# Kernel optimization log

Measured on AMD Instinct MI355X. Metric: run time of the kernel, lower is better.

Reference implementation:

```python
import jax, jax.numpy as jnp
import numpy as np

B, TT, C, H, T = 4, 4096, 1024, 16, 128
K = C // H  # head size (rk and v head sizes equal here)
HEAD_DIV = 8.0  # head_size_divisor
EPS = 1e-5  # GroupNorm eps
LAYER_ID, N_LAYER = 12, 24


def setup_inputs() -> dict:
    key = jax.random.key(0)
    ks = jax.random.split(key, 8)
    r01 = LAYER_ID / (N_LAYER - 1)
    r1a0 = 1.0 - LAYER_ID / N_LAYER
    ddd = (jnp.arange(C, dtype=jnp.float32) / C).reshape(1, 1, C)
    h = jnp.arange(H, dtype=jnp.float32)
    scale = 0.02
    return {
        "xq": jax.random.normal(ks[0], (B, TT, C), jnp.float32),
        "time_mix_k": ddd ** r1a0,
        "time_mix_v": ddd ** r1a0 + 0.3 * r01,
        "time_mix_r": ddd ** (0.5 * r1a0),
        "time_mix_g": ddd ** (0.5 * r1a0),
        "time_decay": -8.0 + 7.0 * (h / (H - 1)) ** (0.7 + 1.3 * r01),
        "time_faaaa": r01 * (1.0 - h / (H - 1)),
        "W_r": jax.random.normal(ks[1], (C, C), jnp.float32) * scale,
        "W_k": jax.random.normal(ks[2], (C, C), jnp.float32) * scale,
        "W_v": jax.random.normal(ks[3], (C, C), jnp.float32) * scale,
        "W_g": jax.random.normal(ks[4], (C, C), jnp.float32) * scale,
        "W_o": jax.random.normal(ks[5], (C, C), jnp.float32) * scale,
        "ln_w": jnp.ones((C,), jnp.float32),
        "ln_b": jnp.zeros((C,), jnp.float32),
    }


def reference(xq, time_mix_k, time_mix_v, time_mix_r, time_mix_g,
              time_decay, time_faaaa, W_r, W_k, W_v, W_g, W_o, ln_w, ln_b):
    x = xq
    B_, TT_, C_ = x.shape
    N = TT_ // T  # number of chunks
    # time shift: xx[:, t] = x[:, t-1], xx[:, 0] = 0
    xx = jnp.pad(x, ((0, 0), (1, 0), (0, 0)))[:, :-1]
    xr = x * time_mix_r + xx * (1 - time_mix_r)
    xk = x * time_mix_k + xx * (1 - time_mix_k)
    xv = x * time_mix_v + xx * (1 - time_mix_v)
    xg = x * time_mix_g + xx * (1 - time_mix_g)
    r = (xr @ W_r.T).reshape(B_, TT_, H, K).transpose(0, 2, 1, 3)  # (B,H,TT,K)
    k = (xk @ W_k.T).reshape(B_, TT_, H, K).transpose(0, 2, 1, 3)
    v = (xv @ W_v.T).reshape(B_, TT_, H, K).transpose(0, 2, 1, 3)
    g = jax.nn.silu(xg @ W_g.T)  # (B,TT,C)

    decay = jnp.exp(-jnp.exp(time_decay))  # (H,)
    u = time_faaaa  # (H,)
    ws = decay ** T  # per-chunk state decay (H,)
    i_idx = jnp.arange(T)
    wb = decay[:, None] ** i_idx                # (H,T): decay^i
    wk = decay[:, None] ** (T - 1 - i_idx)      # (H,T): decay^(T-1-j)
    diff = i_idx[:, None] - i_idx[None, :]      # i - j
    pw = decay[:, None, None] ** jnp.maximum(diff - 1, 0)
    # lower-triangular intra-chunk decay: decay^(i-j-1) for i>j, u on diag
    w_mat = jnp.where(diff > 0, pw, 0.0) + jnp.eye(T, dtype=x.dtype) * u[:, None, None]  # (H,T,T)

    # chunked layout: (N, B, H, T, K)
    rc = r.reshape(B_, H, N, T, K).transpose(2, 0, 1, 3, 4)
    kc = k.reshape(B_, H, N, T, K).transpose(2, 0, 1, 3, 4)
    vc = v.reshape(B_, H, N, T, K).transpose(2, 0, 1, 3, 4)
    s0 = jnp.zeros((B_, H, K, K), x.dtype)

    def step(s, chunk):
        rr, kk, vv = chunk
        att = jnp.einsum('bhik,bhjk->bhij', rr, kk) * w_mat
        out = att @ vv + jnp.einsum('bhik,bhkv->bhiv', rr, s) * wb[None, :, :, None]
        s_new = ws[None, :, None, None] * s + jnp.einsum(
            'bhjk,bhjv->bhkv', kk * wk[None, :, :, None], vv)
        return s_new, out

    _, xo = jax.lax.scan(step, s0, (rc, kc, vc))  # xo: (N,B,H,T,K)
    xo = xo.transpose(1, 0, 3, 2, 4).reshape(B_, TT_, H, K)

    # GroupNorm(H groups) over channels, applied to x / head_size_divisor
    y = xo / HEAD_DIV
    mu = y.mean(-1, keepdims=True)
    var = y.var(-1, keepdims=True)
    y = (y - mu) / jnp.sqrt(var + EPS)
    y = y * ln_w.reshape(H, K) + ln_b.reshape(H, K)
    y = y.reshape(B_, TT_, C_)
    return (y * g) @ W_o.T
```

## Files before the change

kernel.cpp:

```cpp
#include <hip/hip_runtime.h>
#include <hip/hip_bf16.h>
#include <stdint.h>

#define C_DIM 1024
#define H_DIM 16
#define K_DIM 64
#define T_CH 128
#define TT_DIM 4096
#define B_DIM 4
#define N_CH 32
#define M_ROWS 16384

typedef __attribute__((ext_vector_type(8))) __bf16 bf16x8;
typedef __attribute__((ext_vector_type(4))) float floatx4;

__device__ __forceinline__ float bf2f(ushort u) {
  union { uint32_t i; float f; } v; v.i = ((uint32_t)u) << 16; return v.f;
}
__device__ __forceinline__ ushort f2bf(float f) {
  union { float f; uint32_t i; } v; v.f = f;
  return (ushort)((v.i + 0x7fffu + ((v.i >> 16) & 1u)) >> 16);
}

#define GLOAD_LDS16(g, l)                                                     \
  __builtin_amdgcn_global_load_lds(                                           \
      (const __attribute__((address_space(1))) void*)(g),                     \
      (__attribute__((address_space(3))) void*)(l), 16, 0, 0)

__global__ __launch_bounds__(256) void mix_kernel(
    const float* __restrict__ x,
    const float* __restrict__ mk, const float* __restrict__ mv,
    const float* __restrict__ mr, const float* __restrict__ mg,
    ushort* __restrict__ xr, ushort* __restrict__ xk,
    ushort* __restrict__ xv, ushort* __restrict__ xg) {
  long idx = (long)blockIdx.x * 256 + threadIdx.x;
  long e = idx * 4;
  int c = (int)(e & (C_DIM - 1));
  long row = e >> 10;
  int t = (int)(row & (TT_DIM - 1));
  floatx4 xc = *(const floatx4*)(x + e);
  floatx4 xp = {0.f, 0.f, 0.f, 0.f};
  if (t != 0) xp = *(const floatx4*)(x + e - C_DIM);
  floatx4 d = xc - xp;
  floatx4 vk = *(const floatx4*)(mk + c);
  floatx4 vv = *(const floatx4*)(mv + c);
  floatx4 vr = *(const floatx4*)(mr + c);
  floatx4 vg = *(const floatx4*)(mg + c);
  floatx4 ok = xp + d * vk;
  floatx4 ov = xp + d * vv;
  floatx4 orr = xp + d * vr;
  floatx4 og = xp + d * vg;
  union { ushort u[4]; uint2 q; } pk;
#define ST(dst, val)                                                          \
  pk.u[0] = f2bf(val.x); pk.u[1] = f2bf(val.y);                               \
  pk.u[2] = f2bf(val.z); pk.u[3] = f2bf(val.w);                               \
  *(uint2*)((dst) + e) = pk.q;
  ST(xk, ok) ST(xv, ov) ST(xr, orr) ST(xg, og)
#undef ST
}

__global__ __launch_bounds__(256) void wconv_kernel(
    const float* __restrict__ w0, const float* __restrict__ w1,
    const float* __restrict__ w2, const float* __restrict__ w3,
    const float* __restrict__ w4, ushort* __restrict__ o) {
  long idx = (long)blockIdx.x * 256 + threadIdx.x;
  long e = idx * 4;
  int wi = (int)(e >> 20);
  long off = e & ((1L << 20) - 1);
  const float* src = wi == 0 ? w0 : wi == 1 ? w1 : wi == 2 ? w2 : wi == 3 ? w3 : w4;
  floatx4 vv = *(const floatx4*)(src + off);
  union { ushort u[4]; uint2 q; } pk;
  pk.u[0] = f2bf(vv.x); pk.u[1] = f2bf(vv.y);
  pk.u[2] = f2bf(vv.z); pk.u[3] = f2bf(vv.w);
  *(uint2*)(o + e) = pk.q;
}

template <int EPI>
__global__ __launch_bounds__(256) void gemm_bt(
    const ushort* __restrict__ A, const ushort* __restrict__ Bt,
    void* __restrict__ Cout) {
  __shared__ __align__(16) ushort As[2][128 * 32];
  __shared__ __align__(16) ushort Bs[2][128 * 32];
  int tid = threadIdx.x;
  int lane = tid & 63, w = tid >> 6;
  int q = lane >> 4, l16 = lane & 15;
  int wm = w >> 1, wn = w & 1;
  int id = blockIdx.x;
  int bn = (id >> 3) & 7;
  int bm = (id & 7) | ((id >> 6) << 3);

  const ushort* gA0 = A + (long)(bm * 128 + w * 16 + (lane >> 2)) * C_DIM + (lane & 3) * 8;
  const ushort* gA1 = gA0 + 64 * C_DIM;
  const ushort* gB0 = Bt + (long)(bn * 128 + w * 16 + (lane >> 2)) * C_DIM + (lane & 3) * 8;
  const ushort* gB1 = gB0 + 64 * C_DIM;
  ushort* lA0 = As[0] + (w * 16) * 32;
  ushort* lA1 = As[0] + (64 + w * 16) * 32;
  ushort* lB0 = Bs[0] + (w * 16) * 32;
  ushort* lB1 = Bs[0] + (64 + w * 16) * 32;
  ushort* lA0p = As[1] + (w * 16) * 32;
  ushort* lA1p = As[1] + (64 + w * 16) * 32;
  ushort* lB0p = Bs[1] + (w * 16) * 32;
  ushort* lB1p = Bs[1] + (64 + w * 16) * 32;

  floatx4 acc[4][4] = {};

  for (int k0 = 0; k0 < C_DIM; k0 += 64) {
    __syncthreads();
    GLOAD_LDS16(gA0, lA0);
    GLOAD_LDS16(gA1, lA1);
    GLOAD_LDS16(gB0, lB0);
    GLOAD_LDS16(gB1, lB1);
    GLOAD_LDS16(gA0 + 32, lA0p);
    GLOAD_LDS16(gA1 + 32, lA1p);
    GLOAD_LDS16(gB0 + 32, lB0p);
    GLOAD_LDS16(gB1 + 32, lB1p);
    gA0 += 64; gA1 += 64; gB0 += 64; gB1 += 64;
    __syncthreads();
#pragma unroll
    for (int p = 0; p < 2; p++) {
      bf16x8 af[4], bfv[4];
#pragma unroll
      for (int i = 0; i < 4; i++)
        af[i] = *(const bf16x8*)&As[p][(wm * 64 + i * 16 + l16) * 32 + q * 8];
#pragma unroll
      for (int i = 0; i < 4; i++)
        bfv[i] = *(const bf16x8*)&Bs[p][(wn * 64 + i * 16 + l16) * 32 + q * 8];
#pragma unroll
      for (int mi = 0; mi < 4; mi++)
#pragma unroll
        for (int ni = 0; ni < 4; ni++)
          acc[mi][ni] = __builtin_amdgcn_mfma_f32_16x16x32_bf16(
              af[mi], bfv[ni], acc[mi][ni], 0, 0, 0);
    }
  }

  int row0 = bm * 128 + wm * 64 + q * 4;
  int col0 = bn * 128 + wn * 64 + l16;
#pragma unroll
  for (int mi = 0; mi < 4; mi++)
#pragma unroll
    for (int ni = 0; ni < 4; ni++)
#pragma unroll
      for (int rg = 0; rg < 4; rg++) {
        long off = (long)(row0 + mi * 16 + rg) * C_DIM + col0 + ni * 16;
        float val = acc[mi][ni][rg];
        if (EPI == 1) val = val / (1.f + expf(-val));
        if (EPI == 2)
          ((float*)Cout)[off] = val;
        else
          ((ushort*)Cout)[off] = f2bf(val);
      }
}

__global__ __launch_bounds__(256) void chunk_state(
    const ushort* __restrict__ kB, const ushort* __restrict__ vB,
    const float* __restrict__ td, ushort* __restrict__ Zc) {
  __shared__ __align__(16) ushort vt_s[64 * 136];
  __shared__ __align__(16) ushort kwt_s[64 * 136];
  int blk = blockIdx.x;
  int bh = blk >> 5, n = blk & 31;
  int b = bh >> 4, h = bh & 15;
  int tid = threadIdx.x;
  int lane = tid & 63, w = tid >> 6;
  int q = lane >> 4, l16 = lane & 15;
  float etd = expf(td[h]);
  long cbase = ((long)b * TT_DIM + n * T_CH) * C_DIM + h * K_DIM;

#pragma unroll
  for (int it = 0; it < 4; it++) {
    int chunk = it * 256 + tid;
    int row = chunk >> 3;
    int cc = (chunk & 7) * 8;
    long ga = cbase + (long)row * C_DIM + cc;
    uint4 kv4 = *(const uint4*)(kB + ga);
    uint4 vv4 = *(const uint4*)(vB + ga);
    float wkj = expf(-(float)(T_CH - 1 - row) * etd);
    const ushort* kp = (const ushort*)&kv4;
    const ushort* vp = (const ushort*)&vv4;
#pragma unroll
    for (int e2 = 0; e2 < 8; e2++) {
      kwt_s[(cc + e2) * 136 + row] = f2bf(bf2f(kp[e2]) * wkj);
      vt_s[(cc + e2) * 136 + row] = vp[e2];
    }
  }
  __syncthreads();

  floatx4 accZ[4] = {};
#pragma unroll
  for (int js = 0; js < 128; js += 32) {
    bf16x8 av = *(const bf16x8*)&vt_s[(w * 16 + l16) * 136 + q * 8 + js];
    bf16x8 bk3[4];
#pragma unroll
    for (int kt = 0; kt < 4; kt++)
      bk3[kt] = *(const bf16x8*)&kwt_s[(kt * 16 + l16) * 136 + q * 8 + js];
#pragma unroll
    for (int kt = 0; kt < 4; kt++)
      accZ[kt] = __builtin_amdgcn_mfma_f32_16x16x32_bf16(av, bk3[kt], accZ[kt], 0, 0, 0);
  }
  long zbase = (long)blk * 4096;
#pragma unroll
  for (int kt = 0; kt < 4; kt++)
#pragma unroll
    for (int rg = 0; rg < 4; rg++)
      Zc[zbase + (w * 16 + q * 4 + rg) * 64 + kt * 16 + l16] = f2bf(accZ[kt][rg]);
}

__global__ __launch_bounds__(256) void state_scan(
    const ushort* __restrict__ Zc, const float* __restrict__ td,
    ushort* __restrict__ Sb) {
  long tg = (long)blockIdx.x * 256 + threadIdx.x;
  int bh = (int)(tg >> 12);
  int e = (int)(tg & 4095);
  int h = bh & 15;
  float wsf = expf(-128.f * expf(td[h]));
  float s = 0.f;
  long base = (long)bh * N_CH * 4096 + e;
#pragma unroll
  for (int n = 0; n < N_CH; n++) {
    Sb[base + n * 4096] = f2bf(s);
    s = wsf * s + bf2f(Zc[base + n * 4096]);
  }
}

__global__ __launch_bounds__(256) void chunk_out(
    const ushort* __restrict__ rB, const ushort* __restrict__ kB,
    const ushort* __restrict__ vB, const ushort* __restrict__ gBuf,
    const ushort* __restrict__ Sb,
    const float* __restrict__ td, const float* __restrict__ tf,
    const float* __restrict__ lnw, const float* __restrict__ lnb,
    ushort* __restrict__ gy) {
  __shared__ __align__(16) ushort rr_s[128 * 72];
  __shared__ __align__(16) ushort un_s[128 * 136];
  __shared__ __align__(16) ushort vt_s[64 * 136];
  __shared__ __align__(16) ushort z_s[64 * 72];

  int blk = blockIdx.x;
  int bh = blk >> 5, n = blk & 31;
  int b = bh >> 4, h = bh & 15;
  int tid = threadIdx.x;
  int lane = tid & 63, w = tid >> 6;
  int q = lane >> 4, l16 = lane & 15;

  float etd = expf(td[h]);
  float u = tf[h];
  long cbase = ((long)b * TT_DIM + n * T_CH) * C_DIM + h * K_DIM;

#pragma unroll
  for (int it = 0; it < 4; it++) {
    int chunk = it * 256 + tid;
    int row = chunk >> 3;
    int cc = (chunk & 7) * 8;
    long ga = cbase + (long)row * C_DIM + cc;
    *(uint4*)&rr_s[row * 72 + cc] = *(const uint4*)(rB + ga);
    *(uint4*)&un_s[row * 136 + cc] = *(const uint4*)(kB + ga);
    uint4 vv4 = *(const uint4*)(vB + ga);
    const ushort* vp = (const ushort*)&vv4;
#pragma unroll
    for (int e2 = 0; e2 < 8; e2++) vt_s[(cc + e2) * 136 + row] = vp[e2];
  }
  {
    long sbase = (long)blk * 4096;
    int v = tid >> 2, c0 = (tid & 3) * 16;
    *(uint4*)&z_s[v * 72 + c0] = *(const uint4*)(Sb + sbase + v * 64 + c0);
    *(uint4*)&z_s[v * 72 + c0 + 8] = *(const uint4*)(Sb + sbase + v * 64 + c0 + 8);
  }
  __syncthreads();

  floatx4 accA[4][4] = {};
  int ai0 = (w >> 1) * 64, aj0 = (w & 1) * 64;
#pragma unroll
  for (int ks = 0; ks < 64; ks += 32) {
    bf16x8 af[4], bk2[4];
#pragma unroll
    for (int i = 0; i < 4; i++)
      af[i] = *(const bf16x8*)&rr_s[(ai0 + i * 16 + l16) * 72 + q * 8 + ks];
#pragma unroll
    for (int j = 0; j < 4; j++)
      bk2[j] = *(const bf16x8*)&un_s[(aj0 + j * 16 + l16) * 136 + q * 8 + ks];
#pragma unroll
    for (int mi = 0; mi < 4; mi++)
#pragma unroll
      for (int nj = 0; nj < 4; nj++)
        accA[mi][nj] = __builtin_amdgcn_mfma_f32_16x16x32_bf16(
            af[mi], bk2[nj], accA[mi][nj], 0, 0, 0);
  }

  floatx4 accB[2][4] = {};
  int i0 = w * 32;
#pragma unroll
  for (int ks = 0; ks < 64; ks += 32) {
    bf16x8 af2[2], bz[4];
#pragma unroll
    for (int it2 = 0; it2 < 2; it2++)
      af2[it2] = *(const bf16x8*)&rr_s[(i0 + it2 * 16 + l16) * 72 + q * 8 + ks];
#pragma unroll
    for (int vt2 = 0; vt2 < 4; vt2++)
      bz[vt2] = *(const bf16x8*)&z_s[(vt2 * 16 + l16) * 72 + q * 8 + ks];
#pragma unroll
    for (int it2 = 0; it2 < 2; it2++)
#pragma unroll
      for (int vt2 = 0; vt2 < 4; vt2++)
        accB[it2][vt2] = __builtin_amdgcn_mfma_f32_16x16x32_bf16(
            af2[it2], bz[vt2], accB[it2][vt2], 0, 0, 0);
  }
  __syncthreads();

#pragma unroll
  for (int mi = 0; mi < 4; mi++)
#pragma unroll
    for (int nj = 0; nj < 4; nj++)
#pragma unroll
      for (int rg = 0; rg < 4; rg++) {
        int i = ai0 + mi * 16 + q * 4 + rg;
        int j = aj0 + nj * 16 + l16;
        float wv = 0.f;
        if (i > j) wv = expf(-(float)(i - j - 1) * etd);
        else if (i == j) wv = u;
        un_s[i * 136 + j] = f2bf(accA[mi][nj][rg] * wv);
      }
  __syncthreads();

  floatx4 accO[2][4] = {};
#pragma unroll
  for (int js = 0; js < 128; js += 32) {
    bf16x8 af3[2], bv[4];
#pragma unroll
    for (int it2 = 0; it2 < 2; it2++)
      af3[it2] = *(const bf16x8*)&un_s[(i0 + it2 * 16 + l16) * 136 + q * 8 + js];
#pragma unroll
    for (int vt2 = 0; vt2 < 4; vt2++)
      bv[vt2] = *(const bf16x8*)&vt_s[(vt2 * 16 + l16) * 136 + q * 8 + js];
#pragma unroll
    for (int it2 = 0; it2 < 2; it2++)
#pragma unroll
      for (int vt2 = 0; vt2 < 4; vt2++)
        accO[it2][vt2] = __builtin_amdgcn_mfma_f32_16x16x32_bf16(
            af3[it2], bv[vt2], accO[it2][vt2], 0, 0, 0);
  }

#pragma unroll
  for (int it2 = 0; it2 < 2; it2++)
#pragma unroll
    for (int rg = 0; rg < 4; rg++) {
      int i = i0 + it2 * 16 + q * 4 + rg;
      float wbi = expf(-(float)i * etd);
      float vals[4];
      float s1 = 0.f, s2 = 0.f;
#pragma unroll
      for (int vt2 = 0; vt2 < 4; vt2++) {
        float val = accO[it2][vt2][rg] + wbi * accB[it2][vt2][rg];
        vals[vt2] = val; s1 += val; s2 += val * val;
      }
#pragma unroll
      for (int mm = 1; mm < 16; mm <<= 1) {
        s1 += __shfl_xor(s1, mm, 64);
        s2 += __shfl_xor(s2, mm, 64);
      }
      float mu = s1 * (1.f / 64.f);
      float va = s2 * (1.f / 64.f) - mu * mu;
      float rinv = rsqrtf(va + 64.f * 1e-5f);
      long rowg = (long)b * TT_DIM + n * T_CH + i;
#pragma unroll
      for (int vt2 = 0; vt2 < 4; vt2++) {
        int c = h * K_DIM + vt2 * 16 + l16;
        float y = (vals[vt2] - mu) * rinv * lnw[c] + lnb[c];
        float gf = bf2f(gBuf[rowg * C_DIM + c]);
        gy[rowg * C_DIM + c] = f2bf(y * gf);
      }
    }
}

extern "C" void kernel_launch(void* const* d_in, const int* in_sizes, int n_in,
                              void* d_out, int out_size, void* d_ws,
                              size_t ws_size, hipStream_t stream) {
  const float* xq  = (const float*)d_in[0];
  const float* tmk = (const float*)d_in[1];
  const float* tmv = (const float*)d_in[2];
  const float* tmr = (const float*)d_in[3];
  const float* tmg = (const float*)d_in[4];
  const float* td  = (const float*)d_in[5];
  const float* tf  = (const float*)d_in[6];
  const float* Wr  = (const float*)d_in[7];
  const float* Wk  = (const float*)d_in[8];
  const float* Wv  = (const float*)d_in[9];
  const float* Wg  = (const float*)d_in[10];
  const float* Wo  = (const float*)d_in[11];
  const float* lnw = (const float*)d_in[12];
  const float* lnb = (const float*)d_in[13];

  char* ws = (char*)d_ws;
  const size_t BUF = (size_t)M_ROWS * C_DIM * 2;
  ushort* b0 = (ushort*)(ws + 0 * BUF);
  ushort* b1 = (ushort*)(ws + 1 * BUF);
  ushort* b2 = (ushort*)(ws + 2 * BUF);
  ushort* b3 = (ushort*)(ws + 3 * BUF);
  ushort* wcv = (ushort*)(ws + 4 * BUF);
  const ushort* wr_b = wcv;
  const ushort* wk_b = wcv + (1 << 20);
  const ushort* wv_b = wcv + 2 * (1 << 20);
  const ushort* wg_b = wcv + 3 * (1 << 20);
  const ushort* wo_b = wcv + 4 * (1 << 20);
  ushort* Zc = (ushort*)(ws + 4 * BUF + 5 * (2 << 20));
  ushort* Sb = Zc + (size_t)64 * N_CH * 4096;
  ushort* rbuf = (ushort*)d_out;

  mix_kernel<<<16384, 256, 0, stream>>>(xq, tmk, tmv, tmr, tmg, b0, b1, b2, b3);
  wconv_kernel<<<5120, 256, 0, stream>>>(Wr, Wk, Wv, Wg, Wo, wcv);

  gemm_bt<0><<<1024, 256, 0, stream>>>(b0, wr_b, rbuf);
  gemm_bt<0><<<1024, 256, 0, stream>>>(b1, wk_b, b0);
  gemm_bt<0><<<1024, 256, 0, stream>>>(b2, wv_b, b1);
  gemm_bt<1><<<1024, 256, 0, stream>>>(b3, wg_b, b2);

  chunk_state<<<2048, 256, 0, stream>>>(b0, b1, td, Zc);
  state_scan<<<1024, 256, 0, stream>>>(Zc, td, Sb);
  chunk_out<<<2048, 256, 0, stream>>>(rbuf, b0, b1, b2, Sb, td, tf, lnw, lnb, b3);

  gemm_bt<2><<<1024, 256, 0, stream>>>(b3, wo_b, (float*)d_out);
}
```

Measured before the change: 489.8 us.

## Rewrite GEMM as 256x256-tile, 8-wave pipelined kernel with swizzled LDS

Replaces the 128x128 double-buffered GEMM with a 256x256 tile per 512-thread block, using 128KB of LDS in two stages with XOR-swizzled rows to avoid bank conflicts. Global-to-LDS loads for the next K tile are interleaved with quarter-tile MFMA groups under explicit vmcnt/lgkmcnt waits, barriers and setprio, overlapping memory with compute. Block IDs are remapped so concurrently running blocks share A/B panels. The gain is more reuse per loaded byte and better latency hiding, at the cost of 128KB LDS per block, only 256 blocks, and a fragile hand-scheduled sync pattern.

```diff
diff --git a/kernel.cpp b/kernel.cpp
--- a/kernel.cpp
+++ b/kernel.cpp
@@ -75,81 +75,149 @@
   *(uint2*)(o + e) = pk.q;
 }
 
+#define BARX() __builtin_amdgcn_s_barrier()
+#define VMW4() asm volatile("s_waitcnt vmcnt(4)" ::: "memory")
+#define VMW0() asm volatile("s_waitcnt vmcnt(0)" ::: "memory")
+#define LGKW() asm volatile("s_waitcnt lgkmcnt(0)" ::: "memory")
+
 template <int EPI>
-__global__ __launch_bounds__(256) void gemm_bt(
+__global__ __launch_bounds__(512, 2) void gemm_bt(
     const ushort* __restrict__ A, const ushort* __restrict__ Bt,
     void* __restrict__ Cout) {
-  __shared__ __align__(16) ushort As[2][128 * 32];
-  __shared__ __align__(16) ushort Bs[2][128 * 32];
-  int tid = threadIdx.x;
-  int lane = tid & 63, w = tid >> 6;
-  int q = lane >> 4, l16 = lane & 15;
-  int wm = w >> 1, wn = w & 1;
-  int id = blockIdx.x;
-  int bn = (id >> 3) & 7;
-  int bm = (id & 7) | ((id >> 6) << 3);
-
-  const ushort* gA0 = A + (long)(bm * 128 + w * 16 + (lane >> 2)) * C_DIM + (lane & 3) * 8;
-  const ushort* gA1 = gA0 + 64 * C_DIM;
-  const ushort* gB0 = Bt + (long)(bn * 128 + w * 16 + (lane >> 2)) * C_DIM + (lane & 3) * 8;
-  const ushort* gB1 = gB0 + 64 * C_DIM;
-  ushort* lA0 = As[0] + (w * 16) * 32;
-  ushort* lA1 = As[0] + (64 + w * 16) * 32;
-  ushort* lB0 = Bs[0] + (w * 16) * 32;
-  ushort* lB1 = Bs[0] + (64 + w * 16) * 32;
-  ushort* lA0p = As[1] + (w * 16) * 32;
-  ushort* lA1p = As[1] + (64 + w * 16) * 32;
-  ushort* lB0p = Bs[1] + (w * 16) * 32;
-  ushort* lB1p = Bs[1] + (64 + w * 16) * 32;
-
-  floatx4 acc[4][4] = {};
-
-  for (int k0 = 0; k0 < C_DIM; k0 += 64) {
-    __syncthreads();
-    GLOAD_LDS16(gA0, lA0);
-    GLOAD_LDS16(gA1, lA1);
-    GLOAD_LDS16(gB0, lB0);
-    GLOAD_LDS16(gB1, lB1);
-    GLOAD_LDS16(gA0 + 32, lA0p);
-    GLOAD_LDS16(gA1 + 32, lA1p);
-    GLOAD_LDS16(gB0 + 32, lB0p);
-    GLOAD_LDS16(gB1 + 32, lB1p);
-    gA0 += 64; gA1 += 64; gB0 += 64; gB1 += 64;
-    __syncthreads();
-#pragma unroll
-    for (int p = 0; p < 2; p++) {
-      bf16x8 af[4], bfv[4];
-#pragma unroll
-      for (int i = 0; i < 4; i++)
-        af[i] = *(const bf16x8*)&As[p][(wm * 64 + i * 16 + l16) * 32 + q * 8];
-#pragma unroll
-      for (int i = 0; i < 4; i++)
-        bfv[i] = *(const bf16x8*)&Bs[p][(wn * 64 + i * 16 + l16) * 32 + q * 8];
-#pragma unroll
-      for (int mi = 0; mi < 4; mi++)
-#pragma unroll
-        for (int ni = 0; ni < 4; ni++)
-          acc[mi][ni] = __builtin_amdgcn_mfma_f32_16x16x32_bf16(
-              af[mi], bfv[ni], acc[mi][ni], 0, 0, 0);
-    }
-  }
-
-  int row0 = bm * 128 + wm * 64 + q * 4;
-  int col0 = bn * 128 + wn * 64 + l16;
-#pragma unroll
-  for (int mi = 0; mi < 4; mi++)
-#pragma unroll
-    for (int ni = 0; ni < 4; ni++)
-#pragma unroll
-      for (int rg = 0; rg < 4; rg++) {
-        long off = (long)(row0 + mi * 16 + rg) * C_DIM + col0 + ni * 16;
-        float val = acc[mi][ni][rg];
+  __shared__ __align__(16) ushort smem[65536];
+  const int tid = threadIdx.x;
+  const int lane = tid & 63, w = tid >> 6;
+  const int q = lane >> 4, l16 = lane & 15;
+  const int wm = w >> 2, wn = w & 3;
+  const int id = blockIdx.x;
+  const int wg = (id & 7) * 32 + (id >> 3);
+  const int bm = wg >> 2, bn = wg & 3;
+
+  const int r8 = tid >> 3;
+  const int c8 = ((tid & 7) ^ (r8 & 7)) * 8;
+  const ushort* gA = A + (long)(bm * 256 + r8) * C_DIM + c8;
+  const ushort* gB = Bt + (long)(bn * 256 + r8) * C_DIM + c8;
+
+  const char* sB = (const char*)smem;
+  const int arow = (wm * 128 + l16) * 128;
+  const int brow = (wn * 64 + l16) * 128;
+  const int swz = (l16 & 7) << 4;
+  const int csv[2] = {(q << 4) ^ swz, ((4 + q) << 4) ^ swz};
+
+  floatx4 acc[8][4] = {};
+  bf16x8 af[4][2];
+  bf16x8 bfv[4][2];
+
+#define STAGE(ISA, sl, hh, tile)                                              \
+  do {                                                                        \
+    const ushort* g_ = (ISA ? gA : gB) + ((hh) * 131072 + (tile) * 64);       \
+    ushort* l_ = smem + ((ISA ? 0 : 32768) + (sl) * 16384 + (hh) * 8192 +     \
+                         w * 512);                                            \
+    GLOAD_LDS16(g_, l_);                         \
+    GLOAD_LDS16(g_ + 65536, l_ + 4096);                \
+  } while (0)
+
+#define READ_A(sl, qr)                                                        \
+  do {                                                                        \
+    _Pragma("unroll") for (int i_ = 0; i_ < 4; ++i_) {                        \
+      af[i_][0] = *(const bf16x8*)(sB + (sl) * 32768 + arow + (qr) * 8192 +   \
+                                   i_ * 2048 + csv[0]);                       \
+      af[i_][1] = *(const bf16x8*)(sB + (sl) * 32768 + arow + (qr) * 8192 +   \
+                                   i_ * 2048 + csv[1]);                       \
+    }                                                                         \
+  } while (0)
+
+#define READ_B(sl, qc)                                                        \
+  do {                                                                        \
+    _Pragma("unroll") for (int j_ = 0; j_ < 2; ++j_) {                        \
+      bfv[(qc) * 2 + j_][0] = *(const bf16x8*)(sB + 65536 + (sl) * 32768 +    \
+                                               brow + (qc) * 4096 +           \
+                                               j_ * 2048 + csv[0]);           \
+      bfv[(qc) * 2 + j_][1] = *(const bf16x8*)(sB + 65536 + (sl) * 32768 +    \
+                                               brow + (qc) * 4096 +           \
+                                               j_ * 2048 + csv[1]);           \
+    }                                                                         \
+  } while (0)
+
+#define MFMA_Q(qr, qc)                                                        \
+  do {                                                                        \
+    __builtin_amdgcn_s_setprio(1);                                            \
+    _Pragma("unroll") for (int i_ = 0; i_ < 4; ++i_)                          \
+        _Pragma("unroll") for (int j_ = 0; j_ < 2; ++j_) {                    \
+      acc[(qr) * 4 + i_][(qc) * 2 + j_] =                                     \
+          __builtin_amdgcn_mfma_f32_16x16x32_bf16(                            \
+              af[i_][0], bfv[(qc) * 2 + j_][0],                               \
+              acc[(qr) * 4 + i_][(qc) * 2 + j_], 0, 0, 0);                    \
+      acc[(qr) * 4 + i_][(qc) * 2 + j_] =                                     \
+          __builtin_amdgcn_mfma_f32_16x16x32_bf16(                            \
+              af[i_][1], bfv[(qc) * 2 + j_][1],                               \
+              acc[(qr) * 4 + i_][(qc) * 2 + j_], 0, 0, 0);                    \
+    }                                                                         \
+    __builtin_amdgcn_s_setprio(0);                                            \
+  } while (0)
+
+  STAGE(1, 0, 0, 0); STAGE(1, 0, 1, 0);
+  STAGE(0, 0, 0, 0); STAGE(0, 0, 1, 0);
+  STAGE(0, 1, 0, 1); STAGE(0, 1, 1, 1);
+  VMW4();
+  BARX();
+
+#pragma unroll 1
+  for (int i = 0; i < 7; ++i) {
+    const int t1 = 2 * i + 1, tn0 = 2 * i + 2, tn1 = 2 * i + 3;
+    READ_A(0, 0); READ_B(0, 0); STAGE(1, 1, 0, t1);
+    BARX(); MFMA_Q(0, 0); LGKW(); BARX();
+    READ_B(0, 1); STAGE(1, 1, 1, t1);
+    BARX(); MFMA_Q(0, 1); LGKW(); BARX();
+    READ_A(0, 1); STAGE(0, 0, 0, tn0);
+    BARX(); MFMA_Q(1, 0); LGKW(); BARX();
+    STAGE(0, 0, 1, tn0); VMW4();
+    BARX(); MFMA_Q(1, 1); LGKW(); BARX();
+    READ_A(1, 0); READ_B(1, 0); STAGE(1, 0, 0, tn0);
+    BARX(); MFMA_Q(0, 0); LGKW(); BARX();
+    READ_B(1, 1); STAGE(1, 0, 1, tn0);
+    BARX(); MFMA_Q(0, 1); LGKW(); BARX();
+    READ_A(1, 1); STAGE(0, 1, 0, tn1);
+    BARX(); MFMA_Q(1, 0); LGKW(); BARX();
+    STAGE(0, 1, 1, tn1); VMW4();
+    BARX(); MFMA_Q(1, 1); LGKW(); BARX();
+  }
+  READ_A(0, 0); READ_B(0, 0); STAGE(1, 1, 0, 15);
+  BARX(); MFMA_Q(0, 0); LGKW(); BARX();
+  READ_B(0, 1); STAGE(1, 1, 1, 15);
+  BARX(); MFMA_Q(0, 1); LGKW(); BARX();
+  READ_A(0, 1);
+  BARX(); MFMA_Q(1, 0); LGKW(); BARX();
+  VMW0();
+  BARX(); MFMA_Q(1, 1); LGKW(); BARX();
+  READ_A(1, 0); READ_B(1, 0);
+  BARX(); MFMA_Q(0, 0); LGKW(); BARX();
+  READ_B(1, 1);
+  BARX(); MFMA_Q(0, 1); LGKW(); BARX();
+  READ_A(1, 1);
+  BARX(); MFMA_Q(1, 0); LGKW(); BARX();
+  BARX(); MFMA_Q(1, 1);
+
+  const int row0 = bm * 256 + wm * 128 + q * 4;
+  const int col0 = bn * 256 + wn * 64 + l16;
+#pragma unroll
+  for (int fi = 0; fi < 8; ++fi)
+#pragma unroll
+    for (int fj = 0; fj < 4; ++fj)
+#pragma unroll
+      for (int rg = 0; rg < 4; ++rg) {
+        long off = (long)(row0 + fi * 16 + rg) * C_DIM + col0 + fj * 16;
+        float val = acc[fi][fj][rg];
         if (EPI == 1) val = val / (1.f + expf(-val));
         if (EPI == 2)
           ((float*)Cout)[off] = val;
         else
           ((ushort*)Cout)[off] = f2bf(val);
       }
+#undef STAGE
+#undef READ_A
+#undef READ_B
+#undef MFMA_Q
 }
 
 __global__ __launch_bounds__(256) void chunk_state(
@@ -407,14 +475,14 @@
   mix_kernel<<<16384, 256, 0, stream>>>(xq, tmk, tmv, tmr, tmg, b0, b1, b2, b3);
   wconv_kernel<<<5120, 256, 0, stream>>>(Wr, Wk, Wv, Wg, Wo, wcv);
 
-  gemm_bt<0><<<1024, 256, 0, stream>>>(b0, wr_b, rbuf);
-  gemm_bt<0><<<1024, 256, 0, stream>>>(b1, wk_b, b0);
-  gemm_bt<0><<<1024, 256, 0, stream>>>(b2, wv_b, b1);
-  gemm_bt<1><<<1024, 256, 0, stream>>>(b3, wg_b, b2);
+  gemm_bt<0><<<256, 512, 0, stream>>>(b0, wr_b, rbuf);
+  gemm_bt<0><<<256, 512, 0, stream>>>(b1, wk_b, b0);
+  gemm_bt<0><<<256, 512, 0, stream>>>(b2, wv_b, b1);
+  gemm_bt<1><<<256, 512, 0, stream>>>(b3, wg_b, b2);
 
   chunk_state<<<2048, 256, 0, stream>>>(b0, b1, td, Zc);
   state_scan<<<1024, 256, 0, stream>>>(Zc, td, Sb);
   chunk_out<<<2048, 256, 0, stream>>>(rbuf, b0, b1, b2, Sb, td, tf, lnw, lnb, b3);
 
-  gemm_bt<2><<<1024, 256, 0, stream>>>(b3, wo_b, (float*)d_out);
-}
+  gemm_bt<2><<<256, 512, 0, stream>>>(b3, wo_b, (float*)d_out);
+}
```

Measured after the change: 434.9 us. -11.2%, faster.
